# Performance work log

Hardware: AMD Instinct MI355X
Metric: run time of the kernel (lower is better)

Reference implementation:

```python
import jax, jax.numpy as jnp
import numpy as np

N = 100000   # nodes
E = 3200000  # directed edges
IN = 128     # in_channels
H = 16       # hidden_channels
OUT = 2      # out_channels
EPS = 1e-5   # BatchNorm eps


def setup_inputs() -> dict:
    key = jax.random.key(0)
    ks = jax.random.split(key, 16)
    x = jax.random.normal(ks[0], (N, IN), jnp.float32)
    edge_index = jax.random.randint(ks[1], (2, E), 0, N, jnp.int32)

    def lin(k, fan_in, fan_out):
        return jax.random.normal(k, (fan_in, fan_out), jnp.float32) / np.sqrt(fan_in)

    return {
        "x": x,
        "edge_index": edge_index,
        "W1": lin(ks[2], IN, H), "b1": jnp.zeros((H,), jnp.float32),
        "W2": lin(ks[3], H, H), "b2": jnp.zeros((H,), jnp.float32),
        "W3": lin(ks[4], H, H), "b3": jnp.zeros((H,), jnp.float32),
        "gamma1": jnp.ones((H,), jnp.float32), "beta1": jnp.zeros((H,), jnp.float32),
        "gamma2": jnp.ones((H,), jnp.float32), "beta2": jnp.zeros((H,), jnp.float32),
        "Wfc": lin(ks[5], H, OUT), "bfc": jnp.zeros((OUT,), jnp.float32),
    }


def reference(x, edge_index, W1, b1, W2, b2, W3, b3,
              gamma1, beta1, gamma2, beta2, Wfc, bfc):
    src, dst = edge_index[0], edge_index[1]
    # symmetric GCN normalization with self loops: deg includes +1 self loop
    deg = jax.ops.segment_sum(jnp.ones((E,), x.dtype), dst, num_segments=N) + 1.0
    dis = jax.lax.rsqrt(deg)                      # [N]
    norm = dis[src] * dis[dst]                    # [E]

    def gcn_conv(h, W, b):
        hw = h @ W                                # [N, F] dense transform
        msg = norm[:, None] * hw[src]             # gather + scale  [E, F]
        agg = jax.ops.segment_sum(msg, dst, num_segments=N)
        agg = agg + (dis * dis)[:, None] * hw     # self-loop contribution
        return agg + b

    def batch_norm(h, g, be):
        mu = h.mean(axis=0)
        var = h.var(axis=0)
        return (h - mu) * jax.lax.rsqrt(var + EPS) * g + be

    h = batch_norm(jax.nn.relu(gcn_conv(x, W1, b1)), gamma1, beta1)
    # dropout is identity in inference / deterministic reference
    h = batch_norm(jax.nn.relu(gcn_conv(h, W2, b2)), gamma2, beta2)
    h = gcn_conv(h, W3, b3)
    return jax.nn.log_softmax(h @ Wfc + bfc, axis=1)
```

## Files before the change

kernel.cpp:

```cpp
#include <hip/hip_runtime.h>
#include <hip/hip_fp16.h>

#define NN 100000
#define EE 3200000
#define INC 128
#define HC 16
#define BN_EPS 1e-5f

#define NPB 256
#define NBUCK ((NN + NPB - 1) / NPB)
#define CAPU 13440
#define BINSZ ((size_t)(NBUCK + 1) * CAPU)
#define BTILE 8192
#define BGRID ((EE + BTILE - 1) / BTILE)
#define SB_CAP 8960
#define GX32 (NN / 32)
#define GGRID (NN / 8)

#define XSTR 132

__device__ __forceinline__ __half2 bits_to_h2(int v) { __half2 h; *(int*)&h = v; return h; }
__device__ __forceinline__ int h2_to_bits(__half2 h) { return *(int*)&h; }


__global__ void init_all(int* __restrict__ bcursor, float* __restrict__ stats,
                         __half2* __restrict__ hws2) {
    int t = threadIdx.x;
    if (t < NBUCK) bcursor[t] = t * CAPU;
    if (t < 64) stats[t] = 0.f;
    if (t < 8) hws2[(size_t)NN * 8 + t] = __half2(__float2half2_rn(0.f));
}


__global__ __launch_bounds__(512) void build_gemm(const int* __restrict__ src,
                          const int* __restrict__ dst,
                          int* __restrict__ bcursor, unsigned* __restrict__ bin,
                          const float* __restrict__ x, const float* __restrict__ W1,
                          __half2* __restrict__ hw_raw) {
    __shared__ __align__(16) char smem[25792];
    int tid = threadIdx.x;
    if (blockIdx.x >= BGRID) {
        float* Ws = (float*)smem;
        float* xs = (float*)(smem + 8192);
        for (int i = tid; i < INC * HC; i += 512) Ws[i] = W1[i];
        int node0 = (blockIdx.x - BGRID) * 32;
        const float4* xsrc = (const float4*)(x + (size_t)node0 * INC);
        float4* xdst = (float4*)xs;
        for (int i = tid; i < 1024; i += 512) {
            int nl = i >> 5, k4 = i & 31;
            xdst[nl * 33 + k4] = xsrc[i];
        }
        __syncthreads();
        int c = tid & 15;
        int nl = tid >> 4;
        int node = node0 + nl;
        const float* xr = xs + nl * XSTR;
        float sum = 0.f;
#pragma unroll
        for (int k = 0; k < INC; ++k) sum += xr[k] * Ws[k * 16 + c];
        float other = __shfl_xor(sum, 1);
        if ((c & 1) == 0) hw_raw[node * 8 + (c >> 1)] = __floats2half2_rn(sum, other);
        return;
    }
    int* hist1 = (int*)smem;
    int* hist2 = (int*)(smem + 1568);
    int* gbase = (int*)(smem + 3136);
    int* cur1  = (int*)(smem + 4704);
    int* cur2  = (int*)(smem + 6272);
    int g = tid >> 8;
    int* myhist = g ? hist2 : hist1;
    for (int k = tid; k < NBUCK; k += 512) { hist1[k] = 0; hist2[k] = 0; }
    __syncthreads();
    int e0 = blockIdx.x * BTILE;
    int cnt = min(BTILE, EE - e0);
    int n4 = cnt >> 2;
    const int4* d4 = (const int4*)(dst + e0);
    const int4* s4 = (const int4*)(src + e0);
    int4 dvr[4], svr[4];
#pragma unroll
    for (int j = 0; j < 4; ++j) {
        int idx = tid + j * 512;
        if (idx < n4) {
            dvr[j] = d4[idx]; svr[j] = s4[idx];
            atomicAdd(&myhist[dvr[j].x >> 8], 1);
            atomicAdd(&myhist[dvr[j].y >> 8], 1);
            atomicAdd(&myhist[dvr[j].z >> 8], 1);
            atomicAdd(&myhist[dvr[j].w >> 8], 1);
        }
    }
    __syncthreads();
    if (tid < NBUCK) {
        int hv = hist1[tid] + hist2[tid];
        if (hv) gbase[tid] = atomicAdd(&bcursor[tid], hv);
        cur1[tid] = 0; cur2[tid] = 0;
    }
    __syncthreads();
    int* mycur = g ? cur2 : cur1;
#pragma unroll
    for (int j = 0; j < 4; ++j) {
        int idx = tid + j * 512;
        if (idx < n4) {
            int d, s, k, p;
            d = dvr[j].x; s = svr[j].x; k = d >> 8;
            p = gbase[k] + (g ? hist1[k] : 0) + atomicAdd(&mycur[k], 1);
            if (p < k * CAPU + SB_CAP) bin[p] = ((unsigned)(d & 255) << 24) | (unsigned)s;
            d = dvr[j].y; s = svr[j].y; k = d >> 8;
            p = gbase[k] + (g ? hist1[k] : 0) + atomicAdd(&mycur[k], 1);
            if (p < k * CAPU + SB_CAP) bin[p] = ((unsigned)(d & 255) << 24) | (unsigned)s;
            d = dvr[j].z; s = svr[j].z; k = d >> 8;
            p = gbase[k] + (g ? hist1[k] : 0) + atomicAdd(&mycur[k], 1);
            if (p < k * CAPU + SB_CAP) bin[p] = ((unsigned)(d & 255) << 24) | (unsigned)s;
            d = dvr[j].w; s = svr[j].w; k = d >> 8;
            p = gbase[k] + (g ? hist1[k] : 0) + atomicAdd(&mycur[k], 1);
            if (p < k * CAPU + SB_CAP) bin[p] = ((unsigned)(d & 255) << 24) | (unsigned)s;
        }
    }
}


__global__ __launch_bounds__(512) void sort_bucket(const int* __restrict__ bcursor,
                            unsigned* __restrict__ bin,
                            unsigned* __restrict__ rowpack, float* __restrict__ dis,
                            const __half2* __restrict__ hw_raw, __half2* __restrict__ hws2) {
    __shared__ unsigned stg[SB_CAP];
    __shared__ int cnt1[NPB], cnt2[NPB], pos1[NPB], pos2[NPB];
    __shared__ int wsum[4];
    int tid = threadIdx.x;
    int g = tid >> 8;
    int* mycnt = g ? cnt2 : cnt1;
    for (int k = tid; k < NPB; k += 512) { cnt1[k] = 0; cnt2[k] = 0; }
    __syncthreads();
    int b = blockIdx.x;
    int beg = b * CAPU;
    int n = min(bcursor[b] - beg, SB_CAP);
    for (int i = tid; i < n; i += 512) {
        unsigned u = bin[beg + i];
        stg[i] = u;
        atomicAdd(&mycnt[u >> 24], 1);
    }
    __syncthreads();
    int node = b * NPB + tid;
    int tot = 0, ptot = 0, c1 = 0;
    if (tid < NPB) {
        c1 = cnt1[tid];
        tot = c1 + cnt2[tid] + ((node < NN) ? 1 : 0);
        ptot = ((tot + 47) / 48) * 48;
    }
    int lane = tid & 63, wv = tid >> 6;
    int v = ptot;
#pragma unroll
    for (int off = 1; off < 64; off <<= 1) {
        int t = __shfl_up(v, off);
        if (lane >= off) v += t;
    }
    if (wv < 4 && lane == 63) wsum[wv] = v;
    __syncthreads();
    if (tid == 0) {
        int run = 0;
#pragma unroll
        for (int j = 0; j < 4; ++j) { int t = wsum[j]; wsum[j] = run; run += t; }
    }
    __syncthreads();
    int lo = 0;
    unsigned padv = (unsigned)NN << 5;
    if (tid < NPB) {
        lo = v - ptot + wsum[wv];
        int self = (node < NN) ? 1 : 0;
        pos1[tid] = lo + self;
        pos2[tid] = lo + self + c1;
        if (node < NN) {
            rowpack[node] = ((unsigned)min(tot, 511) << 23) | (unsigned)(beg + lo);
            float dv = rsqrtf((float)tot);
            dis[node] = dv;
            __half2 d2 = __float2half2_rn(dv);
            const int4* hr = (const int4*)(hw_raw + (size_t)node * 8);
            int4 a = hr[0], bq = hr[1];
            __half2* ha = (__half2*)&a; __half2* hb = (__half2*)&bq;
#pragma unroll
            for (int j = 0; j < 4; ++j) { ha[j] = __hmul2(ha[j], d2); hb[j] = __hmul2(hb[j], d2); }
            int4* hw = (int4*)(hws2 + (size_t)node * 8);
            hw[0] = a; hw[1] = bq;
            bin[beg + lo] = (unsigned)node << 5;
            for (int i2 = tot; i2 < ptot; ++i2) bin[beg + lo + i2] = padv;
        }
    }
    __syncthreads();
    int* mypos = g ? pos2 : pos1;
    for (int i = tid; i < n; i += 512) {
        unsigned u = stg[i];
        int nl = u >> 24;
        int p = atomicAdd(&mypos[nl], 1);
        bin[beg + p] = (u & 0xFFFFFFu) << 5;
    }
}


__global__ void gemm_bn_h_w(const float* __restrict__ agg, const float* __restrict__ stats,
                            const float* __restrict__ gamma, const float* __restrict__ beta,
                            const float* __restrict__ W, const float* __restrict__ dis,
                            __half2* __restrict__ hws2) {
    __shared__ float Ws[HC * HC];
    __shared__ float sc[HC], sf[HC];
    int tid = threadIdx.x;
    if (tid < HC * HC) Ws[tid] = W[tid];
    if (tid < HC) {
        const float invN = 1.0f / NN;
        float mu = stats[tid] * invN;
        float var = stats[16 + tid] * invN - mu * mu;
        float rs = rsqrtf(var + BN_EPS);
        sc[tid] = gamma[tid] * rs;
        sf[tid] = beta[tid] - mu * gamma[tid] * rs;
    }
    __syncthreads();
    int i = blockIdx.x * 256 + tid;
    if (i >= NN * HC) return;
    int n = i >> 4, c = i & 15;
    const float4* ar = (const float4*)(agg + n * HC);
    float sum = 0.f;
#pragma unroll
    for (int q = 0; q < 4; ++q) {
        float4 v = ar[q];
        int k = q * 4;
        float h0 = v.x * sc[k + 0] + sf[k + 0];
        float h1 = v.y * sc[k + 1] + sf[k + 1];
        float h2 = v.z * sc[k + 2] + sf[k + 2];
        float h3 = v.w * sc[k + 3] + sf[k + 3];
        sum += h0 * Ws[(k + 0) * 16 + c] + h1 * Ws[(k + 1) * 16 + c]
             + h2 * Ws[(k + 2) * 16 + c] + h3 * Ws[(k + 3) * 16 + c];
    }
    sum *= dis[n];
    float other = __shfl_xor(sum, 1);
    if ((c & 1) == 0) hws2[n * 8 + (c >> 1)] = __floats2half2_rn(sum, other);
}


__global__ __launch_bounds__(512) void gcn_gather(const unsigned* __restrict__ rowpack,
                           const unsigned* __restrict__ bin,
                           const __half2* __restrict__ hws2,
                           const float* __restrict__ b, float* __restrict__ agg,
                           float* __restrict__ partials) {
    __shared__ float acc[32];
    int tid = threadIdx.x;
    if (tid < 32) acc[tid] = 0.f;
    __syncthreads();
    int lane = tid & 63;
    int node = blockIdx.x * 8 + (tid >> 6);
    int cq = lane & 3;
    int slot = lane >> 2;
    unsigned rp = rowpack[node];
    int beg = (int)(rp & 0x7FFFFFu);
    int tot = (int)(rp >> 23);
    const char* hbase = (const char*)hws2;
    int e0 = beg + slot;
    unsigned v0 = bin[e0], v1 = bin[e0 + 16], v2 = bin[e0 + 32];
    int2 h0 = *(const int2*)(hbase + (size_t)v0 + cq * 8);
    int2 h1 = *(const int2*)(hbase + (size_t)v1 + cq * 8);
    int2 h2 = *(const int2*)(hbase + (size_t)v2 + cq * 8);
    __half2 accA = __hadd2(__hadd2(bits_to_h2(h0.x), bits_to_h2(h1.x)), bits_to_h2(h2.x));
    __half2 accB = __hadd2(__hadd2(bits_to_h2(h0.y), bits_to_h2(h1.y)), bits_to_h2(h2.y));
    for (int off = 48; off < tot; off += 48) {
        unsigned w0 = bin[e0 + off], w1 = bin[e0 + off + 16], w2 = bin[e0 + off + 32];
        int2 g0 = *(const int2*)(hbase + (size_t)w0 + cq * 8);
        int2 g1 = *(const int2*)(hbase + (size_t)w1 + cq * 8);
        int2 g2 = *(const int2*)(hbase + (size_t)w2 + cq * 8);
        accA = __hadd2(accA, __hadd2(__hadd2(bits_to_h2(g0.x), bits_to_h2(g1.x)), bits_to_h2(g2.x)));
        accB = __hadd2(accB, __hadd2(__hadd2(bits_to_h2(g0.y), bits_to_h2(g1.y)), bits_to_h2(g2.y)));
    }
    int ia = h2_to_bits(accA), ib = h2_to_bits(accB);
#pragma unroll
    for (int d = 4; d < 64; d <<= 1) {
        int oa = __shfl_xor(ia, d), ob = __shfl_xor(ib, d);
        accA = __hadd2(accA, bits_to_h2(oa));
        accB = __hadd2(accB, bits_to_h2(ob));
        ia = h2_to_bits(accA); ib = h2_to_bits(accB);
    }
    if (slot == 0) {
        float d = rsqrtf((float)tot);
        float2 sa = __half22float2(accA), sb = __half22float2(accB);
        float t0 = fmaxf(d * sa.x + b[4 * cq + 0], 0.f);
        float t1 = fmaxf(d * sa.y + b[4 * cq + 1], 0.f);
        float t2 = fmaxf(d * sb.x + b[4 * cq + 2], 0.f);
        float t3 = fmaxf(d * sb.y + b[4 * cq + 3], 0.f);
        float4 r; r.x = t0; r.y = t1; r.z = t2; r.w = t3;
        ((float4*)agg)[node * 4 + cq] = r;
        atomicAdd(&acc[4 * cq + 0], t0);
        atomicAdd(&acc[4 * cq + 1], t1);
        atomicAdd(&acc[4 * cq + 2], t2);
        atomicAdd(&acc[4 * cq + 3], t3);
        atomicAdd(&acc[16 + 4 * cq + 0], t0 * t0);
        atomicAdd(&acc[16 + 4 * cq + 1], t1 * t1);
        atomicAdd(&acc[16 + 4 * cq + 2], t2 * t2);
        atomicAdd(&acc[16 + 4 * cq + 3], t3 * t3);
    }
    __syncthreads();
    if (tid < 32) partials[(size_t)blockIdx.x * 32 + tid] = acc[tid];
}


__global__ void reduce_stats(const float* __restrict__ partials, float* __restrict__ stats) {
    int tid = threadIdx.x;
    const int total = GGRID * 32;
    float a = 0.f;
    int i0 = blockIdx.x * 256 + tid;
    for (int i = i0; i < total; i += gridDim.x * 256) a += partials[i];
    __shared__ float acc[32];
    if (tid < 32) acc[tid] = 0.f;
    __syncthreads();
    atomicAdd(&acc[i0 & 31], a);
    __syncthreads();
    if (tid < 32) atomicAdd(&stats[tid], acc[tid]);
}


__global__ __launch_bounds__(512) void gather_fc(const unsigned* __restrict__ rowpack,
                          const unsigned* __restrict__ bin,
                          const __half2* __restrict__ hws2,
                          const float* __restrict__ b, const float* __restrict__ Wfc,
                          const float* __restrict__ bfc, float* __restrict__ out) {
    int tid = threadIdx.x;
    int lane = tid & 63;
    int node = blockIdx.x * 8 + (tid >> 6);
    int cq = lane & 3;
    int slot = lane >> 2;
    unsigned rp = rowpack[node];
    int beg = (int)(rp & 0x7FFFFFu);
    int tot = (int)(rp >> 23);
    const char* hbase = (const char*)hws2;
    int e0 = beg + slot;
    unsigned v0 = bin[e0], v1 = bin[e0 + 16], v2 = bin[e0 + 32];
    int2 h0 = *(const int2*)(hbase + (size_t)v0 + cq * 8);
    int2 h1 = *(const int2*)(hbase + (size_t)v1 + cq * 8);
    int2 h2 = *(const int2*)(hbase + (size_t)v2 + cq * 8);
    __half2 accA = __hadd2(__hadd2(bits_to_h2(h0.x), bits_to_h2(h1.x)), bits_to_h2(h2.x));
    __half2 accB = __hadd2(__hadd2(bits_to_h2(h0.y), bits_to_h2(h1.y)), bits_to_h2(h2.y));
    for (int off = 48; off < tot; off += 48) {
        unsigned w0 = bin[e0 + off], w1 = bin[e0 + off + 16], w2 = bin[e0 + off + 32];
        int2 g0 = *(const int2*)(hbase + (size_t)w0 + cq * 8);
        int2 g1 = *(const int2*)(hbase + (size_t)w1 + cq * 8);
        int2 g2 = *(const int2*)(hbase + (size_t)w2 + cq * 8);
        accA = __hadd2(accA, __hadd2(__hadd2(bits_to_h2(g0.x), bits_to_h2(g1.x)), bits_to_h2(g2.x)));
        accB = __hadd2(accB, __hadd2(__hadd2(bits_to_h2(g0.y), bits_to_h2(g1.y)), bits_to_h2(g2.y)));
    }
    int ia = h2_to_bits(accA), ib = h2_to_bits(accB);
#pragma unroll
    for (int d = 4; d < 64; d <<= 1) {
        int oa = __shfl_xor(ia, d), ob = __shfl_xor(ib, d);
        accA = __hadd2(accA, bits_to_h2(oa));
        accB = __hadd2(accB, bits_to_h2(ob));
        ia = h2_to_bits(accA); ib = h2_to_bits(accB);
    }
    float z0 = 0.f, z1 = 0.f;
    if (slot == 0) {
        float d = rsqrtf((float)tot);
        float2 sa = __half22float2(accA), sb = __half22float2(accB);
        float v0f = d * sa.x + b[4 * cq + 0];
        float v1f = d * sa.y + b[4 * cq + 1];
        float v2f = d * sb.x + b[4 * cq + 2];
        float v3f = d * sb.y + b[4 * cq + 3];
        int k = 4 * cq;
        z0 = v0f * Wfc[(k + 0) * 2 + 0] + v1f * Wfc[(k + 1) * 2 + 0]
           + v2f * Wfc[(k + 2) * 2 + 0] + v3f * Wfc[(k + 3) * 2 + 0];
        z1 = v0f * Wfc[(k + 0) * 2 + 1] + v1f * Wfc[(k + 1) * 2 + 1]
           + v2f * Wfc[(k + 2) * 2 + 1] + v3f * Wfc[(k + 3) * 2 + 1];
    }
    z0 += __shfl_xor(z0, 1); z1 += __shfl_xor(z1, 1);
    z0 += __shfl_xor(z0, 2); z1 += __shfl_xor(z1, 2);
    if (lane == 0) {
        z0 += bfc[0]; z1 += bfc[1];
        float m = fmaxf(z0, z1);
        float lse = m + logf(expf(z0 - m) + expf(z1 - m));
        out[node * 2 + 0] = z0 - lse;
        out[node * 2 + 1] = z1 - lse;
    }
}


extern "C" void kernel_launch(void* const* d_in, const int* in_sizes, int n_in,
                              void* d_out, int out_size, void* d_ws, size_t ws_size,
                              hipStream_t stream) {
    const float* x    = (const float*)d_in[0];
    const int*   ei   = (const int*)d_in[1];
    const int*   src  = ei;
    const int*   dstp = ei + EE;
    const float* W1   = (const float*)d_in[2];
    const float* b1   = (const float*)d_in[3];
    const float* W2   = (const float*)d_in[4];
    const float* b2   = (const float*)d_in[5];
    const float* W3   = (const float*)d_in[6];
    const float* b3   = (const float*)d_in[7];
    const float* g1   = (const float*)d_in[8];
    const float* be1  = (const float*)d_in[9];
    const float* g2   = (const float*)d_in[10];
    const float* be2  = (const float*)d_in[11];
    const float* Wfc  = (const float*)d_in[12];
    const float* bfc  = (const float*)d_in[13];
    float* out = (float*)d_out;

    char* p = (char*)d_ws;
    unsigned* bin   = (unsigned*)p;             p += BINSZ * 4;
    __half2* hws2   = (__half2*)p;              p += (size_t)(NN + 1) * HC * 2;
    __half2* hw_raw = (__half2*)p;              p += (size_t)NN * HC * 2;
    float*  agg     = (float*)p;                p += (size_t)NN * HC * 4;
    float*  dis     = (float*)p;                p += (size_t)NN * 4;
    unsigned* rowpack=(unsigned*)p;             p += (size_t)NN * 4;
    float*  partials= (float*)p;                p += (size_t)GGRID * 32 * 4;
    int*    bcursor = (int*)p;                  p += NBUCK * 4;
    float*  stats1  = (float*)p;                p += 32 * 4;
    float*  stats2  = (float*)p;                p += 32 * 4;

    const int TB = 256;
    const int gNH = (NN * HC + TB - 1) / TB;

    init_all<<<1, 512, 0, stream>>>(bcursor, stats1, hws2);
    build_gemm<<<BGRID + GX32, 512, 0, stream>>>(src, dstp, bcursor, bin, x, W1, hw_raw);
    sort_bucket<<<NBUCK, 512, 0, stream>>>(bcursor, bin, rowpack, dis, hw_raw, hws2);

    gcn_gather<<<GGRID, 512, 0, stream>>>(rowpack, bin, hws2, b1, agg, partials);
    reduce_stats<<<128, 256, 0, stream>>>(partials, stats1);

    gemm_bn_h_w<<<gNH, TB, 0, stream>>>(agg, stats1, g1, be1, W2, dis, hws2);
    gcn_gather<<<GGRID, 512, 0, stream>>>(rowpack, bin, hws2, b2, agg, partials);
    reduce_stats<<<128, 256, 0, stream>>>(partials, stats2);

    gemm_bn_h_w<<<gNH, TB, 0, stream>>>(agg, stats2, g2, be2, W3, dis, hws2);
    gather_fc<<<GGRID, 512, 0, stream>>>(rowpack, bin, hws2, b3, Wfc, bfc, out);
}
```

Before: 223.3 us.

## Split fused bin/GEMM kernel and pad bucket cursors to separate cache lines

Splits the combined edge-binning and x@W1 kernel into two separate launches, with the GEMM using 256-thread blocks of 16 nodes so it no longer inherits the 512-thread shared-memory footprint. Bucket cursor counters are padded with a stride of 16 ints so global atomics from different buckets do not contend on the same cache line. This adds an extra kernel launch and removes the overlap the fused kernel had between the GEMM and binning work.

```diff
diff --git a/kernel.cpp b/kernel.cpp
--- a/kernel.cpp
+++ b/kernel.cpp
@@ -14,8 +14,9 @@
 #define BTILE 8192
 #define BGRID ((EE + BTILE - 1) / BTILE)
 #define SB_CAP 8960
-#define GX32 (NN / 32)
+#define GX16 (NN / 16)
 #define GGRID (NN / 8)
+#define CSTR 16
 
 #define XSTR 132
 
@@ -25,48 +26,18 @@
 
 __global__ void init_all(int* __restrict__ bcursor, float* __restrict__ stats,
                          __half2* __restrict__ hws2) {
-    int t = threadIdx.x;
-    if (t < NBUCK) bcursor[t] = t * CAPU;
+    int t = blockIdx.x * 512 + threadIdx.x;
+    if (t < NBUCK) bcursor[t * CSTR] = t * CAPU;
     if (t < 64) stats[t] = 0.f;
     if (t < 8) hws2[(size_t)NN * 8 + t] = __half2(__float2half2_rn(0.f));
 }
 
 
-__global__ __launch_bounds__(512) void build_gemm(const int* __restrict__ src,
+__global__ __launch_bounds__(512) void bin_edges(const int* __restrict__ src,
                           const int* __restrict__ dst,
-                          int* __restrict__ bcursor, unsigned* __restrict__ bin,
-                          const float* __restrict__ x, const float* __restrict__ W1,
-                          __half2* __restrict__ hw_raw) {
-    __shared__ __align__(16) char smem[25792];
-    int tid = threadIdx.x;
-    if (blockIdx.x >= BGRID) {
-        float* Ws = (float*)smem;
-        float* xs = (float*)(smem + 8192);
-        for (int i = tid; i < INC * HC; i += 512) Ws[i] = W1[i];
-        int node0 = (blockIdx.x - BGRID) * 32;
-        const float4* xsrc = (const float4*)(x + (size_t)node0 * INC);
-        float4* xdst = (float4*)xs;
-        for (int i = tid; i < 1024; i += 512) {
-            int nl = i >> 5, k4 = i & 31;
-            xdst[nl * 33 + k4] = xsrc[i];
-        }
-        __syncthreads();
-        int c = tid & 15;
-        int nl = tid >> 4;
-        int node = node0 + nl;
-        const float* xr = xs + nl * XSTR;
-        float sum = 0.f;
-#pragma unroll
-        for (int k = 0; k < INC; ++k) sum += xr[k] * Ws[k * 16 + c];
-        float other = __shfl_xor(sum, 1);
-        if ((c & 1) == 0) hw_raw[node * 8 + (c >> 1)] = __floats2half2_rn(sum, other);
-        return;
-    }
-    int* hist1 = (int*)smem;
-    int* hist2 = (int*)(smem + 1568);
-    int* gbase = (int*)(smem + 3136);
-    int* cur1  = (int*)(smem + 4704);
-    int* cur2  = (int*)(smem + 6272);
+                          int* __restrict__ bcursor, unsigned* __restrict__ bin) {
+    __shared__ int hist1[NBUCK], hist2[NBUCK], gbase[NBUCK], cur1[NBUCK], cur2[NBUCK];
+    int tid = threadIdx.x;
     int g = tid >> 8;
     int* myhist = g ? hist2 : hist1;
     for (int k = tid; k < NBUCK; k += 512) { hist1[k] = 0; hist2[k] = 0; }
@@ -91,7 +62,7 @@
     __syncthreads();
     if (tid < NBUCK) {
         int hv = hist1[tid] + hist2[tid];
-        if (hv) gbase[tid] = atomicAdd(&bcursor[tid], hv);
+        if (hv) gbase[tid] = atomicAdd(&bcursor[tid * CSTR], hv);
         cur1[tid] = 0; cur2[tid] = 0;
     }
     __syncthreads();
@@ -118,6 +89,32 @@
 }
 
 
+__global__ void gemm_x_w1(const float* __restrict__ x, const float* __restrict__ W1,
+                          __half2* __restrict__ hw_raw) {
+    __shared__ float Ws[INC * HC];
+    __shared__ float xs[16 * XSTR];
+    int tid = threadIdx.x;
+    for (int i = tid; i < INC * HC; i += 256) Ws[i] = W1[i];
+    int node0 = blockIdx.x * 16;
+    const float4* xsrc = (const float4*)(x + (size_t)node0 * INC);
+    float4* xdst = (float4*)xs;
+    for (int i = tid; i < 512; i += 256) {
+        int nl = i >> 5, k4 = i & 31;
+        xdst[nl * 33 + k4] = xsrc[i];
+    }
+    __syncthreads();
+    int c = tid & 15;
+    int nl = tid >> 4;
+    int node = node0 + nl;
+    const float* xr = xs + nl * XSTR;
+    float sum = 0.f;
+#pragma unroll
+    for (int k = 0; k < INC; ++k) sum += xr[k] * Ws[k * 16 + c];
+    float other = __shfl_xor(sum, 1);
+    if ((c & 1) == 0) hw_raw[node * 8 + (c >> 1)] = __floats2half2_rn(sum, other);
+}
+
+
 __global__ __launch_bounds__(512) void sort_bucket(const int* __restrict__ bcursor,
                             unsigned* __restrict__ bin,
                             unsigned* __restrict__ rowpack, float* __restrict__ dis,
@@ -132,7 +129,7 @@
     __syncthreads();
     int b = blockIdx.x;
     int beg = b * CAPU;
-    int n = min(bcursor[b] - beg, SB_CAP);
+    int n = min(bcursor[b * CSTR] - beg, SB_CAP);
     for (int i = tid; i < n; i += 512) {
         unsigned u = bin[beg + i];
         stg[i] = u;
@@ -404,7 +401,7 @@
     float*  dis     = (float*)p;                p += (size_t)NN * 4;
     unsigned* rowpack=(unsigned*)p;             p += (size_t)NN * 4;
     float*  partials= (float*)p;                p += (size_t)GGRID * 32 * 4;
-    int*    bcursor = (int*)p;                  p += NBUCK * 4;
+    int*    bcursor = (int*)p;                  p += NBUCK * CSTR * 4;
     float*  stats1  = (float*)p;                p += 32 * 4;
     float*  stats2  = (float*)p;                p += 32 * 4;
 
@@ -412,7 +409,8 @@
     const int gNH = (NN * HC + TB - 1) / TB;
 
     init_all<<<1, 512, 0, stream>>>(bcursor, stats1, hws2);
-    build_gemm<<<BGRID + GX32, 512, 0, stream>>>(src, dstp, bcursor, bin, x, W1, hw_raw);
+    gemm_x_w1<<<GX16, TB, 0, stream>>>(x, W1, hw_raw);
+    bin_edges<<<BGRID, 512, 0, stream>>>(src, dstp, bcursor, bin);
     sort_bucket<<<NBUCK, 512, 0, stream>>>(bcursor, bin, rowpack, dis, hw_raw, hws2);
 
     gcn_gather<<<GGRID, 512, 0, stream>>>(rowpack, bin, hws2, b1, agg, partials);
```

New measurement: 232.2 us. 4.0% more time.
